# Optimization experiments

Hardware: AMD Instinct MI355X
Metric: run time of the kernel (lower is better)

Reference implementation:

```python
import jax, jax.numpy as jnp
import numpy as np

GAMMA = 0.5  # RBF bandwidth, matches init_kwargs gamma


def setup_inputs() -> dict:
    key = jax.random.key(0)
    x = jax.random.normal(key, (8192, 64), dtype=jnp.float32)
    return {"x": x}


def reference(x):
    # Gram[i, j] = exp(-gamma * ||x_i - x_j||^2), computed fully batched.
    # ||xi - xj||^2 = ||xi||^2 + ||xj||^2 - 2 <xi, xj>
    sq = jnp.sum(x * x, axis=-1)                      # [n]
    d2 = sq[:, None] + sq[None, :] - 2.0 * (x @ x.T)  # [n, n]
    d2 = jnp.maximum(d2, 0.0)                         # numerical floor
    out = jnp.exp(-GAMMA * d2)                        # [n, n]
    n = x.shape[0]
    return out.reshape(n, -1)
```

## Files before the change

### kernel.cpp

```cpp
#include <hip/hip_runtime.h>


#define GAMMA 0.5f

typedef __attribute__((ext_vector_type(8))) short short8;
typedef __attribute__((ext_vector_type(4))) float f32x4;

__device__ __forceinline__ unsigned short bf16_rne(float f) {
    unsigned u = __builtin_bit_cast(unsigned, f);
    u += 0x7fffu + ((u >> 16) & 1u);
    return (unsigned short)(u >> 16);
}

__global__ __launch_bounds__(256) void split_kernel(const float* __restrict__ x,
                                                    unsigned short* __restrict__ Xh,
                                                    unsigned short* __restrict__ Xl,
                                                    float* __restrict__ sq) {
    int tid = blockIdx.x * 256 + threadIdx.x;
    int row = tid >> 4, c4 = tid & 15;
    float4 v = ((const float4*)x)[tid];
    float e[4] = {v.x, v.y, v.z, v.w};
    unsigned short h[4], l[4];
    float s = 0.f;
    #pragma unroll
    for (int i = 0; i < 4; ++i) {
        h[i] = bf16_rne(e[i]);
        float hf = __builtin_bit_cast(float, (unsigned)h[i] << 16);
        l[i] = bf16_rne(e[i] - hf);
        s = fmaf(e[i], e[i], s);
    }
    int rr = row & 127;
    size_t base = (size_t)(row >> 7) * 16384;
    int b = (rr * 128 + c4 * 8) ^ ((rr & 7) << 4);
    uint2 hw = {(unsigned)h[0] | ((unsigned)h[1] << 16), (unsigned)h[2] | ((unsigned)h[3] << 16)};
    uint2 lw = {(unsigned)l[0] | ((unsigned)l[1] << 16), (unsigned)l[2] | ((unsigned)l[3] << 16)};
    *(uint2*)((char*)Xh + base + b) = hw;
    *(uint2*)((char*)Xl + base + b) = lw;
    s += __shfl_xor(s, 1); s += __shfl_xor(s, 2);
    s += __shfl_xor(s, 4); s += __shfl_xor(s, 8);
    if (c4 == 0) sq[row] = s;
}

__global__ __launch_bounds__(256) void rbf_mfma2(const unsigned short* __restrict__ Xh,
                                                 const unsigned short* __restrict__ Xl,
                                                 const float* __restrict__ sq,
                                                 float* __restrict__ out, int N) {
    __shared__ unsigned short Ah[8192], Al[8192], Bh[8192], Bl[8192];

    const int tid = threadIdx.x;
    const int i0 = blockIdx.y * 128, j0 = blockIdx.x * 128;
    const int w = tid >> 6, lane = tid & 63;
    const int fr = lane & 15, kg = lane >> 4;
    const int wr = (w >> 1) * 64, wc = (w & 1) * 64;

    {
        uint4* l4[4] = {(uint4*)Ah, (uint4*)Al, (uint4*)Bh, (uint4*)Bl};
        const uint4* g4[4] = {(const uint4*)(Xh + (size_t)i0 * 64),
                              (const uint4*)(Xl + (size_t)i0 * 64),
                              (const uint4*)(Xh + (size_t)j0 * 64),
                              (const uint4*)(Xl + (size_t)j0 * 64)};
        #pragma unroll
        for (int b = 0; b < 4; ++b)
            #pragma unroll
            for (int t = 0; t < 4; ++t)
                l4[b][t * 256 + tid] = g4[b][t * 256 + tid];
    }
    __syncthreads();

    f32x4 acc[4][4];
    #pragma unroll
    for (int p = 0; p < 4; ++p)
        #pragma unroll
        for (int q = 0; q < 4; ++q) acc[p][q] = (f32x4)(0.f);

    #pragma unroll
    for (int ks = 0; ks < 2; ++ks) {
        const int kb = ks * 64 + kg * 16;
        short8 ah[4], al[4], bh[4], bl[4];
        #pragma unroll
        for (int p = 0; p < 4; ++p) {
            int R = wr + p * 16 + fr;
            int off = (R * 128 + kb) ^ ((R & 7) << 4);
            ah[p] = *(const short8*)((const char*)Ah + off);
            al[p] = *(const short8*)((const char*)Al + off);
        }
        #pragma unroll
        for (int q = 0; q < 4; ++q) {
            int R = wc + q * 16 + fr;
            int off = (R * 128 + kb) ^ ((R & 7) << 4);
            bh[q] = *(const short8*)((const char*)Bh + off);
            bl[q] = *(const short8*)((const char*)Bl + off);
        }
        #pragma unroll
        for (int p = 0; p < 4; ++p)
            #pragma unroll
            for (int q = 0; q < 4; ++q)
                acc[p][q] = __builtin_amdgcn_mfma_f32_16x16x32_bf16(bh[q], ah[p], acc[p][q], 0, 0, 0);
        #pragma unroll
        for (int p = 0; p < 4; ++p)
            #pragma unroll
            for (int q = 0; q < 4; ++q)
                acc[p][q] = __builtin_amdgcn_mfma_f32_16x16x32_bf16(bl[q], ah[p], acc[p][q], 0, 0, 0);
        #pragma unroll
        for (int p = 0; p < 4; ++p)
            #pragma unroll
            for (int q = 0; q < 4; ++q)
                acc[p][q] = __builtin_amdgcn_mfma_f32_16x16x32_bf16(bh[q], al[p], acc[p][q], 0, 0, 0);
    }

    #pragma unroll
    for (int p = 0; p < 4; ++p) {
        int ri = wr + p * 16 + fr;
        float sa = sq[i0 + ri];
        float* rowp = out + (size_t)(i0 + ri) * N + j0;
        #pragma unroll
        for (int q = 0; q < 4; ++q) {
            int c = wc + q * 16 + kg * 4;
            float4 sb = *(const float4*)&sq[j0 + c];
            f32x4 a = acc[p][q];
            float4 r;
            r.x = __expf(-GAMMA * fmaxf(fmaf(-2.f, a[0], sa + sb.x), 0.f));
            r.y = __expf(-GAMMA * fmaxf(fmaf(-2.f, a[1], sa + sb.y), 0.f));
            r.z = __expf(-GAMMA * fmaxf(fmaf(-2.f, a[2], sa + sb.z), 0.f));
            r.w = __expf(-GAMMA * fmaxf(fmaf(-2.f, a[3], sa + sb.w), 0.f));
            *(float4*)(rowp + c) = r;
        }
    }
}

extern "C" void kernel_launch(void* const* d_in, const int* in_sizes, int n_in,
                              void* d_out, int out_size, void* d_ws, size_t ws_size,
                              hipStream_t stream) {
    (void)n_in; (void)ws_size; (void)out_size;
    const float* x = (const float*)d_in[0];
    float* out = (float*)d_out;
    const int K = 64;
    const int N = in_sizes[0] / K;

    unsigned short* Xh = (unsigned short*)d_ws;
    unsigned short* Xl = Xh + (size_t)N * K;
    float* sq = (float*)(Xl + (size_t)N * K);

    split_kernel<<<dim3(N * K / 4 / 256), dim3(256), 0, stream>>>(x, Xh, Xl, sq);
    rbf_mfma2<<<dim3(N / 128, N / 128), dim3(256), 0, stream>>>(Xh, Xl, sq, out, N);
}
```

Measured before the change: 65.86 us.

## Make blocks persistent over eight column tiles with register-prefetched B tiles

Each block now keeps its A row tile in shared memory and walks eight consecutive column tiles. The next B tile is prefetched into registers while the current tile's MFMA and exp/store epilogue run. The grid shrinks from 4096 blocks to 512, and launch bounds request two blocks per CU. This amortizes the A load and hides B load latency, but with so few blocks it may not fill the CUs, and the store-bound epilogue is serialized within each block.

```diff
diff --git a/kernel.cpp b/kernel.cpp
--- a/kernel.cpp
+++ b/kernel.cpp
@@ -41,89 +41,112 @@
     if (c4 == 0) sq[row] = s;
 }
 
-__global__ __launch_bounds__(256) void rbf_mfma2(const unsigned short* __restrict__ Xh,
-                                                 const unsigned short* __restrict__ Xl,
-                                                 const float* __restrict__ sq,
-                                                 float* __restrict__ out, int N) {
+__global__ __launch_bounds__(256, 2) void rbf_mfma4(const unsigned short* __restrict__ Xh,
+                                                    const unsigned short* __restrict__ Xl,
+                                                    const float* __restrict__ sq,
+                                                    float* __restrict__ out, int N) {
     __shared__ unsigned short Ah[8192], Al[8192], Bh[8192], Bl[8192];
 
     const int tid = threadIdx.x;
-    const int i0 = blockIdx.y * 128, j0 = blockIdx.x * 128;
+    const int bi  = blockIdx.x >> 3;
+    const int bj0 = (blockIdx.x & 7) * 8;
+    const int i0  = bi * 128;
+
     const int w = tid >> 6, lane = tid & 63;
     const int fr = lane & 15, kg = lane >> 4;
     const int wr = (w >> 1) * 64, wc = (w & 1) * 64;
 
     {
-        uint4* l4[4] = {(uint4*)Ah, (uint4*)Al, (uint4*)Bh, (uint4*)Bl};
-        const uint4* g4[4] = {(const uint4*)(Xh + (size_t)i0 * 64),
-                              (const uint4*)(Xl + (size_t)i0 * 64),
-                              (const uint4*)(Xh + (size_t)j0 * 64),
-                              (const uint4*)(Xl + (size_t)j0 * 64)};
+        const uint4* gh = (const uint4*)(Xh + (size_t)i0 * 64);
+        const uint4* gl = (const uint4*)(Xl + (size_t)i0 * 64);
         #pragma unroll
-        for (int b = 0; b < 4; ++b)
+        for (int t = 0; t < 4; ++t) {
+            ((uint4*)Ah)[t * 256 + tid] = gh[t * 256 + tid];
+            ((uint4*)Al)[t * 256 + tid] = gl[t * 256 + tid];
+        }
+    }
+    uint4 ph[4], pl[4];
+    {
+        const uint4* gh = (const uint4*)(Xh + (size_t)bj0 * 128 * 64);
+        const uint4* gl = (const uint4*)(Xl + (size_t)bj0 * 128 * 64);
+        #pragma unroll
+        for (int t = 0; t < 4; ++t) { ph[t] = gh[t * 256 + tid]; pl[t] = gl[t * 256 + tid]; }
+    }
+
+    for (int tj = 0; tj < 8; ++tj) {
+        const int j0 = (bj0 + tj) * 128;
+        __syncthreads();
+        #pragma unroll
+        for (int t = 0; t < 4; ++t) {
+            ((uint4*)Bh)[t * 256 + tid] = ph[t];
+            ((uint4*)Bl)[t * 256 + tid] = pl[t];
+        }
+        __syncthreads();
+        if (tj < 7) {
+            const uint4* gh = (const uint4*)(Xh + (size_t)(j0 + 128) * 64);
+            const uint4* gl = (const uint4*)(Xl + (size_t)(j0 + 128) * 64);
             #pragma unroll
-            for (int t = 0; t < 4; ++t)
-                l4[b][t * 256 + tid] = g4[b][t * 256 + tid];
-    }
-    __syncthreads();
+            for (int t = 0; t < 4; ++t) { ph[t] = gh[t * 256 + tid]; pl[t] = gl[t * 256 + tid]; }
+        }
 
-    f32x4 acc[4][4];
-    #pragma unroll
-    for (int p = 0; p < 4; ++p)
-        #pragma unroll
-        for (int q = 0; q < 4; ++q) acc[p][q] = (f32x4)(0.f);
-
-    #pragma unroll
-    for (int ks = 0; ks < 2; ++ks) {
-        const int kb = ks * 64 + kg * 16;
-        short8 ah[4], al[4], bh[4], bl[4];
-        #pragma unroll
-        for (int p = 0; p < 4; ++p) {
-            int R = wr + p * 16 + fr;
-            int off = (R * 128 + kb) ^ ((R & 7) << 4);
-            ah[p] = *(const short8*)((const char*)Ah + off);
-            al[p] = *(const short8*)((const char*)Al + off);
-        }
-        #pragma unroll
-        for (int q = 0; q < 4; ++q) {
-            int R = wc + q * 16 + fr;
-            int off = (R * 128 + kb) ^ ((R & 7) << 4);
-            bh[q] = *(const short8*)((const char*)Bh + off);
-            bl[q] = *(const short8*)((const char*)Bl + off);
-        }
+        f32x4 acc[4][4];
         #pragma unroll
         for (int p = 0; p < 4; ++p)
             #pragma unroll
-            for (int q = 0; q < 4; ++q)
-                acc[p][q] = __builtin_amdgcn_mfma_f32_16x16x32_bf16(bh[q], ah[p], acc[p][q], 0, 0, 0);
+            for (int q = 0; q < 4; ++q) acc[p][q] = (f32x4)(0.f);
+
         #pragma unroll
-        for (int p = 0; p < 4; ++p)
+        for (int ks = 0; ks < 2; ++ks) {
+            const int kb = ks * 64 + kg * 16;
+            short8 ah[4], al[4], bh[4], bl[4];
             #pragma unroll
-            for (int q = 0; q < 4; ++q)
-                acc[p][q] = __builtin_amdgcn_mfma_f32_16x16x32_bf16(bl[q], ah[p], acc[p][q], 0, 0, 0);
+            for (int p = 0; p < 4; ++p) {
+                int R = wr + p * 16 + fr;
+                int off = (R * 128 + kb) ^ ((R & 7) << 4);
+                ah[p] = *(const short8*)((const char*)Ah + off);
+                al[p] = *(const short8*)((const char*)Al + off);
+            }
+            #pragma unroll
+            for (int q = 0; q < 4; ++q) {
+                int R = wc + q * 16 + fr;
+                int off = (R * 128 + kb) ^ ((R & 7) << 4);
+                bh[q] = *(const short8*)((const char*)Bh + off);
+                bl[q] = *(const short8*)((const char*)Bl + off);
+            }
+            #pragma unroll
+            for (int p = 0; p < 4; ++p)
+                #pragma unroll
+                for (int q = 0; q < 4; ++q)
+                    acc[p][q] = __builtin_amdgcn_mfma_f32_16x16x32_bf16(bh[q], ah[p], acc[p][q], 0, 0, 0);
+            #pragma unroll
+            for (int p = 0; p < 4; ++p)
+                #pragma unroll
+                for (int q = 0; q < 4; ++q)
+                    acc[p][q] = __builtin_amdgcn_mfma_f32_16x16x32_bf16(bl[q], ah[p], acc[p][q], 0, 0, 0);
+            #pragma unroll
+            for (int p = 0; p < 4; ++p)
+                #pragma unroll
+                for (int q = 0; q < 4; ++q)
+                    acc[p][q] = __builtin_amdgcn_mfma_f32_16x16x32_bf16(bh[q], al[p], acc[p][q], 0, 0, 0);
+        }
+
         #pragma unroll
-        for (int p = 0; p < 4; ++p)
+        for (int p = 0; p < 4; ++p) {
+            int ri = wr + p * 16 + fr;
+            float sa = sq[i0 + ri];
+            float* rowp = out + (size_t)(i0 + ri) * N + j0;
             #pragma unroll
-            for (int q = 0; q < 4; ++q)
-                acc[p][q] = __builtin_amdgcn_mfma_f32_16x16x32_bf16(bh[q], al[p], acc[p][q], 0, 0, 0);
-    }
-
-    #pragma unroll
-    for (int p = 0; p < 4; ++p) {
-        int ri = wr + p * 16 + fr;
-        float sa = sq[i0 + ri];
-        float* rowp = out + (size_t)(i0 + ri) * N + j0;
-        #pragma unroll
-        for (int q = 0; q < 4; ++q) {
-            int c = wc + q * 16 + kg * 4;
-            float4 sb = *(const float4*)&sq[j0 + c];
-            f32x4 a = acc[p][q];
-            float4 r;
-            r.x = __expf(-GAMMA * fmaxf(fmaf(-2.f, a[0], sa + sb.x), 0.f));
-            r.y = __expf(-GAMMA * fmaxf(fmaf(-2.f, a[1], sa + sb.y), 0.f));
-            r.z = __expf(-GAMMA * fmaxf(fmaf(-2.f, a[2], sa + sb.z), 0.f));
-            r.w = __expf(-GAMMA * fmaxf(fmaf(-2.f, a[3], sa + sb.w), 0.f));
-            *(float4*)(rowp + c) = r;
+            for (int q = 0; q < 4; ++q) {
+                int c = wc + q * 16 + kg * 4;
+                float4 sb = *(const float4*)&sq[j0 + c];
+                f32x4 a = acc[p][q];
+                float4 r;
+                r.x = __expf(-GAMMA * fmaxf(fmaf(-2.f, a[0], sa + sb.x), 0.f));
+                r.y = __expf(-GAMMA * fmaxf(fmaf(-2.f, a[1], sa + sb.y), 0.f));
+                r.z = __expf(-GAMMA * fmaxf(fmaf(-2.f, a[2], sa + sb.z), 0.f));
+                r.w = __expf(-GAMMA * fmaxf(fmaf(-2.f, a[3], sa + sb.w), 0.f));
+                *(float4*)(rowp + c) = r;
+            }
         }
     }
 }
@@ -142,5 +165,5 @@
     float* sq = (float*)(Xl + (size_t)N * K);
 
     split_kernel<<<dim3(N * K / 4 / 256), dim3(256), 0, stream>>>(x, Xh, Xl, sq);
-    rbf_mfma2<<<dim3(N / 128, N / 128), dim3(256), 0, stream>>>(Xh, Xl, sq, out, N);
+    rbf_mfma4<<<dim3((N / 128) * 8), dim3(256), 0, stream>>>(Xh, Xl, sq, out, N);
 }
```

After: 99.41 us. 1.51x slower.
